# Kernel optimization log

Hardware: AMD Instinct MI355X
Metric: run time of the kernel (lower is better)

The kernel has to match this reference:

```python
import jax, jax.numpy as jnp
import numpy as np

N = 50000      # nodes
E = 800000     # edges (avg degree 16)
F_IN = 32
H = 64         # hidden_features
E_DIM = 16     # edge_dim
C_OUT = 40
L = 2          # num_layers
G = 64         # graphs in batch
BN_EPS = 1e-5
GEN_EPS = 1e-7  # PyG GENConv message eps


def setup_inputs() -> dict:
    key = jax.random.key(0)
    ks = jax.random.split(key, 12)
    s = 0.05
    inp = {}
    inp["x"] = jax.random.normal(ks[0], (N, F_IN), jnp.float32)
    inp["edge_index"] = jax.random.randint(ks[1], (2, E), 0, N)
    inp["edge_attr"] = jax.random.normal(ks[2], (E, E_DIM), jnp.float32)
    inp["batch"] = jnp.sort(jax.random.randint(ks[3], (N,), 0, G))
    # input linear
    inp["lin_in_w"] = jax.random.normal(ks[4], (F_IN, H), jnp.float32) * s
    inp["lin_in_b"] = jnp.zeros((H,), jnp.float32)
    # per-layer DeepGCNLayer norm (BatchNorm affine)
    inp["norm_gamma"] = jnp.ones((L, H), jnp.float32)
    inp["norm_beta"] = jnp.zeros((L, H), jnp.float32)
    # per-layer GENConv params
    inp["edge_w"] = jax.random.normal(ks[5], (L, E_DIM, H), jnp.float32) * s
    inp["edge_b"] = jnp.zeros((L, H), jnp.float32)
    inp["t"] = jnp.ones((L,), jnp.float32)  # learned softmax temperature
    inp["mlp_w1"] = jax.random.normal(ks[6], (L, H, 2 * H), jnp.float32) * s
    inp["mlp_b1"] = jnp.zeros((L, 2 * H), jnp.float32)
    inp["mlp_gamma"] = jnp.ones((L, 2 * H), jnp.float32)
    inp["mlp_beta"] = jnp.zeros((L, 2 * H), jnp.float32)
    inp["mlp_w2"] = jax.random.normal(ks[7], (L, 2 * H, H), jnp.float32) * s
    inp["mlp_b2"] = jnp.zeros((L, H), jnp.float32)
    # output linear
    inp["lin_out_w"] = jax.random.normal(ks[8], (H, C_OUT), jnp.float32) * s
    inp["lin_out_b"] = jnp.zeros((C_OUT,), jnp.float32)
    return inp


def _batch_norm(x, gamma, beta):
    mu = jnp.mean(x, axis=0)
    var = jnp.var(x, axis=0)
    return (x - mu) * jax.lax.rsqrt(var + BN_EPS) * gamma + beta


def _gen_conv(x, src, dst, e_emb, t, w1, b1, g1, be1, w2, b2):
    # message: relu(x_j + edge_emb) + eps   -> [E, H]
    m = jax.nn.relu(x[src] + e_emb) + GEN_EPS
    # softmax aggregation over destination neighborhoods with temperature t
    logits = m * t
    seg_max = jax.ops.segment_max(logits, dst, num_segments=N)      # [N, H]
    ex = jnp.exp(logits - seg_max[dst])                              # [E, H]
    denom = jax.ops.segment_sum(ex, dst, num_segments=N)            # [N, H]
    agg = jax.ops.segment_sum(ex * m, dst, num_segments=N) / (denom + 1e-16)
    # root add, then GENConv MLP: Linear(H,2H) -> BN -> ReLU -> Linear(2H,H)
    out = agg + x
    h = out @ w1 + b1
    h = jax.nn.relu(_batch_norm(h, g1, be1))
    return h @ w2 + b2


def reference(x, edge_index, edge_attr, batch, lin_in_w, lin_in_b,
              norm_gamma, norm_beta, edge_w, edge_b, t,
              mlp_w1, mlp_b1, mlp_gamma, mlp_beta, mlp_w2, mlp_b2,
              lin_out_w, lin_out_b):
    src, dst = edge_index[0], edge_index[1]
    h = x @ lin_in_w + lin_in_b                                      # [N, H]
    for l in range(L):
        # DeepGCNLayer res+ : norm -> act -> (dropout p=0) -> conv, residual add
        z = jax.nn.relu(_batch_norm(h, norm_gamma[l], norm_beta[l]))
        e_emb = edge_attr @ edge_w[l] + edge_b[l]                    # [E, H]
        c = _gen_conv(z, src, dst, e_emb, t[l], mlp_w1[l], mlp_b1[l],
                      mlp_gamma[l], mlp_beta[l], mlp_w2[l], mlp_b2[l])
        h = h + c
    # global mean pool per graph
    sums = jax.ops.segment_sum(h, batch, num_segments=G)             # [G, H]
    counts = jax.ops.segment_sum(jnp.ones((N, 1), h.dtype), batch, num_segments=G)
    pooled = sums / jnp.maximum(counts, 1.0)
    out = jax.nn.relu(pooled) @ lin_out_w + lin_out_b                # [G, C_OUT]
    return out
```

## Files before the change

kernel.cpp:

```cpp
#include <hip/hip_runtime.h>

#define N_NODES 50000
#define N_EDGES 800000
#define F_INP   32
#define HDIM    64
#define EDIM    16
#define COUT    40
#define NGRAPH  64
#define LDS_STRIDE 18

__global__ void hist_kernel(const int* __restrict__ dst, int* __restrict__ cnt, int E) {
    int e = blockIdx.x * 256 + threadIdx.x;
    if (e < E) atomicAdd(&cnt[dst[e]], 1);
}

__global__ void scan_part_kernel(const int* __restrict__ cnt, int* __restrict__ bsum, int n) {
    __shared__ int red[256];
    int tid = threadIdx.x;
    int idx = blockIdx.x * 256 + tid;
    red[tid] = (idx < n) ? cnt[idx] : 0;
    __syncthreads();
    for (int off = 128; off > 0; off >>= 1) {
        if (tid < off) red[tid] += red[tid + off];
        __syncthreads();
    }
    if (tid == 0) bsum[blockIdx.x] = red[0];
}

__global__ void scan_top_kernel(int* __restrict__ bsum, int nb) {
    __shared__ int tmp[256];
    int tid = threadIdx.x;
    int v = (tid < nb) ? bsum[tid] : 0;
    tmp[tid] = v;
    __syncthreads();
    for (int off = 1; off < 256; off <<= 1) {
        int x = (tid >= off) ? tmp[tid - off] : 0;
        __syncthreads();
        tmp[tid] += x;
        __syncthreads();
    }
    if (tid < nb) bsum[tid] = tmp[tid] - v;
}

__global__ void scan_apply_kernel(const int* __restrict__ cnt, const int* __restrict__ bsum,
                                  int* __restrict__ offsets, int* __restrict__ cursor, int n) {
    __shared__ int tmp[256];
    int tid = threadIdx.x;
    int idx = blockIdx.x * 256 + tid;
    int v = (idx < n) ? cnt[idx] : 0;
    tmp[tid] = v;
    __syncthreads();
    for (int off = 1; off < 256; off <<= 1) {
        int x = (tid >= off) ? tmp[tid - off] : 0;
        __syncthreads();
        tmp[tid] += x;
        __syncthreads();
    }
    int excl = tmp[tid] - v + bsum[blockIdx.x];
    if (idx < n) { offsets[idx] = excl; cursor[idx] = excl; }
    if (idx == n - 1) offsets[n] = excl + v;
}

__global__ void scatter_kernel(const int* __restrict__ dst, const int* __restrict__ src,
                               int* __restrict__ cursor, int* __restrict__ sorted,
                               int* __restrict__ dsts, int* __restrict__ srcs, int E) {
    int e = blockIdx.x * 256 + threadIdx.x;
    if (e < E) {
        int d = dst[e];
        int p = atomicAdd(&cursor[d], 1);
        sorted[p] = e;
        dsts[p]   = d;
        srcs[p]   = src[e];
    }
}

__global__ void gstart_kernel(const int* __restrict__ batch, int* __restrict__ gstart,
                              int N, int G) {
    int n = blockIdx.x * 256 + threadIdx.x;
    if (n >= N) return;
    int g  = batch[n];
    int gp = (n == 0) ? -1 : batch[n - 1];
    for (int gg = gp + 1; gg <= g; gg++) gstart[gg] = n;
    if (n == N - 1) {
        for (int gg = g + 1; gg <= G; gg++) gstart[gg] = N;
    }
}

__global__ void lin_in_kernel(const float* __restrict__ x, const float* __restrict__ W,
                              const float* __restrict__ b, float* __restrict__ h, int N) {
    int tid = threadIdx.x;
    int c = tid & 63;
    float w[F_INP];
#pragma unroll
    for (int k = 0; k < F_INP; k++) w[k] = W[k * HDIM + c];
    int node = blockIdx.x * 4 + (tid >> 6);
    if (node >= N) return;
    const float4* xr = (const float4*)(x + (size_t)node * F_INP);
    float acc = b[c];
#pragma unroll
    for (int k4 = 0; k4 < F_INP / 4; k4++) {
        float4 xv = xr[k4];
        acc += xv.x * w[k4 * 4 + 0] + xv.y * w[k4 * 4 + 1]
             + xv.z * w[k4 * 4 + 2] + xv.w * w[k4 * 4 + 3];
    }
    h[(size_t)node * HDIM + c] = acc;
}

template <int C>
__global__ void bn_stats_kernel(const float* __restrict__ x, float* __restrict__ stats, int N) {
    const int RPB = 256 / C;
    int tid = threadIdx.x;
    int c = tid % C;
    int row0 = blockIdx.x * RPB + tid / C;
    int stride = gridDim.x * RPB;
    float s = 0.f, ss = 0.f;
    for (int r = row0; r < N; r += stride) {
        float v = x[(size_t)r * C + c];
        s += v; ss += v * v;
    }
    __shared__ float ls[256], lss[256];
    ls[tid] = s; lss[tid] = ss;
    __syncthreads();
    if (tid < C) {
        for (int k = 1; k < RPB; k++) { s += ls[tid + k * C]; ss += lss[tid + k * C]; }
        atomicAdd(&stats[c], s);
        atomicAdd(&stats[C + c], ss);
    }
}

__global__ __launch_bounds__(256) void edge_agg_kernel(
        const float* __restrict__ h, const float* __restrict__ ea,
        const int* __restrict__ sorted, const int* __restrict__ dsts,
        const int* __restrict__ srcs,
        const float* __restrict__ We, const float* __restrict__ be,
        const float* __restrict__ tptr, const float* __restrict__ stats,
        const float* __restrict__ gamma, const float* __restrict__ beta,
        float* __restrict__ num, float* __restrict__ den) {
    __shared__ float sA[4 * 64 * LDS_STRIDE];
    int tid = threadIdx.x;
    int c  = tid & 63;
    int wv = tid >> 6;
    float inv = 1.0f / (float)N_NODES;
    float mu  = stats[c] * inv;
    float var = stats[HDIM + c] * inv - mu * mu;
    float sc  = rsqrtf(var + 1e-5f) * gamma[c];
    float sb  = beta[c] - mu * sc;
    float w[EDIM];
#pragma unroll
    for (int k = 0; k < EDIM; k++) w[k] = We[k * HDIM + c];
    float bc = be[c];
    float tl2 = (*tptr) * 1.4426950408889634f;

    int p = (blockIdx.x * 4 + wv) * 64 + c;
    int d_own = dsts[p];
    int s_own = srcs[p];
    int e     = sorted[p];
    float* myrow = &sA[(wv * 64 + c) * LDS_STRIDE];
    {
        const float4* ar = (const float4*)(ea + (size_t)e * EDIM);
        float4 a0 = ar[0], a1 = ar[1], a2 = ar[2], a3 = ar[3];
        myrow[0]=a0.x;  myrow[1]=a0.y;  myrow[2]=a0.z;  myrow[3]=a0.w;
        myrow[4]=a1.x;  myrow[5]=a1.y;  myrow[6]=a1.z;  myrow[7]=a1.w;
        myrow[8]=a2.x;  myrow[9]=a2.y;  myrow[10]=a2.z; myrow[11]=a2.w;
        myrow[12]=a3.x; myrow[13]=a3.y; myrow[14]=a3.z; myrow[15]=a3.w;
    }
    __syncthreads();

    const float* wrow = &sA[(size_t)wv * 64 * LDS_STRIDE];
    float nacc = 0.f, dacc = 0.f;
    int cur_d = __builtin_amdgcn_readlane(d_own, 0);
    for (int jj = 0; jj < 64; jj += 8) {
        float hv[8];
#pragma unroll
        for (int u = 0; u < 8; u++) {
            int su = __builtin_amdgcn_readlane(s_own, jj + u);
            hv[u] = h[(size_t)su * HDIM + c];
        }
#pragma unroll
        for (int u = 0; u < 8; u++) {
            int du = __builtin_amdgcn_readlane(d_own, jj + u);
            if (du != cur_d) {
                atomicAdd(&num[(size_t)cur_d * HDIM + c], nacc);
                atomicAdd(&den[(size_t)cur_d * HDIM + c], dacc);
                nacc = 0.f; dacc = 0.f;
                cur_d = du;
            }
            const float2* arow = (const float2*)&wrow[(jj + u) * LDS_STRIDE];
            float acc = bc;
#pragma unroll
            for (int k2 = 0; k2 < 8; k2++) {
                float2 av = arow[k2];
                acc += av.x * w[2 * k2] + av.y * w[2 * k2 + 1];
            }
            float zv = fmaxf(hv[u] * sc + sb, 0.f);
            float m  = fmaxf(zv + acc, 0.f) + 1e-7f;
            float ex = exp2f(m * tl2);
            dacc += ex;
            nacc += ex * m;
        }
    }
    atomicAdd(&num[(size_t)cur_d * HDIM + c], nacc);
    atomicAdd(&den[(size_t)cur_d * HDIM + c], dacc);
}

__global__ __launch_bounds__(256) void mlp1_kernel(
        float* __restrict__ num, float* __restrict__ den,
        const float* __restrict__ h, const float* __restrict__ stats,
        const float* __restrict__ gamma, const float* __restrict__ beta,
        const float* __restrict__ W1, const float* __restrict__ b1,
        float* __restrict__ h1, int N) {
    __shared__ float sW[HDIM * 128];
    __shared__ float srow[32 * 65];
    int tid = threadIdx.x;
    for (int i = tid; i < HDIM * 128; i += 256) sW[i] = W1[i];
    int base = blockIdx.x * 32;
    {
        int cc = tid & 63;
        float inv = 1.0f / (float)N_NODES;
        float mu  = stats[cc] * inv;
        float var = stats[HDIM + cc] * inv - mu * mu;
        float rs  = rsqrtf(var + 1e-5f);
        float ga  = gamma[cc], bb = beta[cc];
        for (int i = tid; i < 32 * HDIM; i += 256) {
            int r = i >> 6;
            int node = base + r;
            float v = 0.f;
            if (node < N) {
                size_t idx = (size_t)node * HDIM + cc;
                float hv = h[idx];
                float z  = fmaxf((hv - mu) * rs * ga + bb, 0.f);
                float nu = num[idx], de = den[idx];
                num[idx] = 0.f; den[idx] = 0.f;
                v = nu / (de + 1e-16f) + z;
            }
            srow[r * 65 + cc] = v;
        }
    }
    __syncthreads();
    int tx = tid & 31;
    int ty = tid >> 5;
    float acc[4][4];
    float b0 = b1[4 * tx], bb1 = b1[4 * tx + 1], b2v = b1[4 * tx + 2], b3 = b1[4 * tx + 3];
#pragma unroll
    for (int j = 0; j < 4; j++) { acc[j][0] = b0; acc[j][1] = bb1; acc[j][2] = b2v; acc[j][3] = b3; }
#pragma unroll 8
    for (int k = 0; k < HDIM; k++) {
        float4 wv = *(const float4*)&sW[k * 128 + 4 * tx];
        float r0 = srow[(ty * 4 + 0) * 65 + k];
        float r1 = srow[(ty * 4 + 1) * 65 + k];
        float r2 = srow[(ty * 4 + 2) * 65 + k];
        float r3 = srow[(ty * 4 + 3) * 65 + k];
        acc[0][0] += r0 * wv.x; acc[0][1] += r0 * wv.y; acc[0][2] += r0 * wv.z; acc[0][3] += r0 * wv.w;
        acc[1][0] += r1 * wv.x; acc[1][1] += r1 * wv.y; acc[1][2] += r1 * wv.z; acc[1][3] += r1 * wv.w;
        acc[2][0] += r2 * wv.x; acc[2][1] += r2 * wv.y; acc[2][2] += r2 * wv.z; acc[2][3] += r2 * wv.w;
        acc[3][0] += r3 * wv.x; acc[3][1] += r3 * wv.y; acc[3][2] += r3 * wv.z; acc[3][3] += r3 * wv.w;
    }
#pragma unroll
    for (int j = 0; j < 4; j++) {
        int node = base + ty * 4 + j;
        if (node < N)
            *(float4*)&h1[(size_t)node * 128 + 4 * tx] =
                make_float4(acc[j][0], acc[j][1], acc[j][2], acc[j][3]);
    }
}

__global__ __launch_bounds__(256) void mlp2_kernel(
        const float* __restrict__ h1, const float* __restrict__ stats,
        const float* __restrict__ mg, const float* __restrict__ mb,
        const float* __restrict__ W2, const float* __restrict__ b2,
        float* __restrict__ h, int N) {
    __shared__ float sW[128 * HDIM];
    __shared__ float sact[32 * 129];
    __shared__ float sbn[4 * 128];
    int tid = threadIdx.x;
    for (int i = tid; i < 128 * HDIM; i += 256) sW[i] = W2[i];
    if (tid < 128) {
        float inv = 1.0f / (float)N;
        float mu  = stats[tid] * inv;
        float var = stats[128 + tid] * inv - mu * mu;
        sbn[tid]       = mu;
        sbn[128 + tid] = rsqrtf(var + 1e-5f);
        sbn[256 + tid] = mg[tid];
        sbn[384 + tid] = mb[tid];
    }
    __syncthreads();
    int base = blockIdx.x * 32;
    for (int i = tid; i < 32 * 128; i += 256) {
        int r = i >> 7, o = i & 127;
        int node = base + r;
        float v = 0.f;
        if (node < N) {
            v = h1[(size_t)node * 128 + o];
            v = fmaxf((v - sbn[o]) * sbn[128 + o] * sbn[256 + o] + sbn[384 + o], 0.f);
        }
        sact[r * 129 + o] = v;
    }
    __syncthreads();
    int tx = tid & 15;
    int ty = tid >> 4;
    float acc[2][4];
    float b0 = b2[4 * tx], bb1 = b2[4 * tx + 1], b2v = b2[4 * tx + 2], b3 = b2[4 * tx + 3];
    acc[0][0] = b0; acc[0][1] = bb1; acc[0][2] = b2v; acc[0][3] = b3;
    acc[1][0] = b0; acc[1][1] = bb1; acc[1][2] = b2v; acc[1][3] = b3;
#pragma unroll 8
    for (int k = 0; k < 128; k++) {
        float4 wv = *(const float4*)&sW[k * HDIM + 4 * tx];
        float r0 = sact[(ty * 2 + 0) * 129 + k];
        float r1 = sact[(ty * 2 + 1) * 129 + k];
        acc[0][0] += r0 * wv.x; acc[0][1] += r0 * wv.y; acc[0][2] += r0 * wv.z; acc[0][3] += r0 * wv.w;
        acc[1][0] += r1 * wv.x; acc[1][1] += r1 * wv.y; acc[1][2] += r1 * wv.z; acc[1][3] += r1 * wv.w;
    }
#pragma unroll
    for (int j = 0; j < 2; j++) {
        int node = base + ty * 2 + j;
        if (node < N) {
            float4* p = (float4*)&h[(size_t)node * HDIM + 4 * tx];
            float4 old = *p;
            *p = make_float4(old.x + acc[j][0], old.y + acc[j][1],
                             old.z + acc[j][2], old.w + acc[j][3]);
        }
    }
}

__global__ void pool_out_kernel(const float* __restrict__ h, const int* __restrict__ gstart,
                                const float* __restrict__ Wo, const float* __restrict__ bo,
                                float* __restrict__ out, int N) {
    __shared__ float sp[HDIM];
    __shared__ float red[256];
    __shared__ float sW[HDIM * COUT];
    int g = blockIdx.x;
    int tid = threadIdx.x;
    for (int i = tid; i < HDIM * COUT; i += 256) sW[i] = Wo[i];
    int beg = gstart[g], end = gstart[g + 1];
    int c = tid & 63, r0 = tid >> 6;
    float s = 0.f;
    for (int r = beg + r0; r < end; r += 4) s += h[(size_t)r * HDIM + c];
    red[tid] = s;
    __syncthreads();
    if (tid < HDIM) {
        s = red[tid] + red[tid + 64] + red[tid + 128] + red[tid + 192];
        float cnt = (float)(end - beg);
        float pooled = s / fmaxf(cnt, 1.0f);
        sp[tid] = fmaxf(pooled, 0.0f);
    }
    __syncthreads();
    if (tid < COUT) {
        float acc = bo[tid];
#pragma unroll
        for (int k = 0; k < HDIM; k++) acc += sp[k] * sW[k * COUT + tid];
        out[g * COUT + tid] = acc;
    }
}

extern "C" void kernel_launch(void* const* d_in, const int* in_sizes, int n_in,
                              void* d_out, int out_size, void* d_ws, size_t ws_size,
                              hipStream_t stream) {
    (void)in_sizes; (void)n_in; (void)out_size; (void)ws_size;
    const float* x          = (const float*)d_in[0];
    const int*   eidx       = (const int*)  d_in[1];
    const float* eattr      = (const float*)d_in[2];
    const int*   batch      = (const int*)  d_in[3];
    const float* lin_in_w   = (const float*)d_in[4];
    const float* lin_in_b   = (const float*)d_in[5];
    const float* norm_gamma = (const float*)d_in[6];
    const float* norm_beta  = (const float*)d_in[7];
    const float* edge_w     = (const float*)d_in[8];
    const float* edge_b     = (const float*)d_in[9];
    const float* tparam     = (const float*)d_in[10];
    const float* mlp_w1     = (const float*)d_in[11];
    const float* mlp_b1     = (const float*)d_in[12];
    const float* mlp_gamma  = (const float*)d_in[13];
    const float* mlp_beta   = (const float*)d_in[14];
    const float* mlp_w2     = (const float*)d_in[15];
    const float* mlp_b2     = (const float*)d_in[16];
    const float* lin_out_w  = (const float*)d_in[17];
    const float* lin_out_b  = (const float*)d_in[18];
    float* out = (float*)d_out;

    const int* src = eidx;
    const int* dst = eidx + N_EDGES;

    char* ws = (char*)d_ws;
    size_t off = 0;
    auto alloc = [&](size_t bytes) -> char* {
        char* p = ws + off;
        off = (off + bytes + 255) & ~(size_t)255;
        return p;
    };
    int*   cnt     = (int*)  alloc((size_t)N_NODES * 4);
    float* statsA0 = (float*)alloc(128 * 4);
    float* statsB0 = (float*)alloc(256 * 4);
    float* statsA1 = (float*)alloc(128 * 4);
    float* statsB1 = (float*)alloc(256 * 4);
    size_t zero_bytes = off;
    int*   bsum    = (int*)  alloc(256 * 4);
    int*   offsets = (int*)  alloc((size_t)(N_NODES + 1) * 4);
    int*   cursor  = (int*)  alloc((size_t)N_NODES * 4);
    int*   sorted  = (int*)  alloc((size_t)N_EDGES * 4);
    int*   dsts    = (int*)  alloc((size_t)N_EDGES * 4);
    int*   srcs    = (int*)  alloc((size_t)N_EDGES * 4);
    int*   gstart  = (int*)  alloc((size_t)(NGRAPH + 1) * 4);
    float* h       = (float*)alloc((size_t)N_NODES * HDIM * 4);
    float* num     = (float*)alloc((size_t)N_NODES * HDIM * 4);
    float* den     = (float*)alloc((size_t)N_NODES * HDIM * 4);
    float* h1      = (float*)alloc((size_t)N_NODES * 2 * HDIM * 4);

    hipMemsetAsync(d_ws, 0, zero_bytes, stream);
    hipMemsetAsync(num, 0, (size_t)N_NODES * HDIM * 4 * 2, stream);

    const int NB = (N_NODES + 255) / 256;
    hist_kernel      <<<(N_EDGES + 255) / 256, 256, 0, stream>>>(dst, cnt, N_EDGES);
    scan_part_kernel <<<NB, 256, 0, stream>>>(cnt, bsum, N_NODES);
    scan_top_kernel  <<<1, 256, 0, stream>>>(bsum, NB);
    scan_apply_kernel<<<NB, 256, 0, stream>>>(cnt, bsum, offsets, cursor, N_NODES);
    scatter_kernel   <<<(N_EDGES + 255) / 256, 256, 0, stream>>>(dst, src, cursor, sorted, dsts, srcs, N_EDGES);
    gstart_kernel    <<<NB, 256, 0, stream>>>(batch, gstart, N_NODES, NGRAPH);
    lin_in_kernel    <<<(N_NODES + 3) / 4, 256, 0, stream>>>(x, lin_in_w, lin_in_b, h, N_NODES);

    const int AGG_BLOCKS = N_EDGES / 256;

    float* statsA[2] = { statsA0, statsA1 };
    float* statsB[2] = { statsB0, statsB1 };
    for (int l = 0; l < 2; l++) {
        bn_stats_kernel<64><<<256, 256, 0, stream>>>(h, statsA[l], N_NODES);
        edge_agg_kernel<<<AGG_BLOCKS, 256, 0, stream>>>(
            h, eattr, sorted, dsts, srcs,
            edge_w + (size_t)l * EDIM * HDIM, edge_b + l * HDIM,
            tparam + l, statsA[l], norm_gamma + l * HDIM, norm_beta + l * HDIM,
            num, den);
        mlp1_kernel<<<(N_NODES + 31) / 32, 256, 0, stream>>>(
            num, den, h, statsA[l], norm_gamma + l * HDIM, norm_beta + l * HDIM,
            mlp_w1 + (size_t)l * HDIM * 2 * HDIM, mlp_b1 + l * 2 * HDIM, h1, N_NODES);
        bn_stats_kernel<128><<<256, 256, 0, stream>>>(h1, statsB[l], N_NODES);
        mlp2_kernel<<<(N_NODES + 31) / 32, 256, 0, stream>>>(
            h1, statsB[l], mlp_gamma + l * 2 * HDIM, mlp_beta + l * 2 * HDIM,
            mlp_w2 + (size_t)l * 2 * HDIM * HDIM, mlp_b2 + l * HDIM, h, N_NODES);
    }
    pool_out_kernel<<<NGRAPH, 256, 0, stream>>>(h, gstart, lin_out_w, lin_out_b, out, N_NODES);
}
```

Measured before the change: 654.4 us.

## Pack sorted edge metadata into int4 and precompute segment boundary ballot mask

The scatter kernel now writes one int4 record per sorted edge (dst, src, edge id) instead of three separate int arrays, so the aggregation kernel gets its metadata with a single vector load. Segment boundaries are found once per wavefront with a shuffle and ballot, which replaces the per-edge readlane comparison. The edge-embedding dot product uses packed 2-wide float vectors to encourage packed FMA, and the outer loop is kept rolled to limit register pressure. The int4 layout carries an unused padding word, which adds write traffic in the scatter kernel.

```diff
diff --git a/kernel.cpp b/kernel.cpp
--- a/kernel.cpp
+++ b/kernel.cpp
@@ -9,6 +9,8 @@
 #define NGRAPH  64
 #define LDS_STRIDE 18
 
+typedef float v2f __attribute__((ext_vector_type(2)));
+
 __global__ void hist_kernel(const int* __restrict__ dst, int* __restrict__ cnt, int E) {
     int e = blockIdx.x * 256 + threadIdx.x;
     if (e < E) atomicAdd(&cnt[dst[e]], 1);
@@ -62,15 +64,12 @@
 }
 
 __global__ void scatter_kernel(const int* __restrict__ dst, const int* __restrict__ src,
-                               int* __restrict__ cursor, int* __restrict__ sorted,
-                               int* __restrict__ dsts, int* __restrict__ srcs, int E) {
+                               int* __restrict__ cursor, int4* __restrict__ edge4, int E) {
     int e = blockIdx.x * 256 + threadIdx.x;
     if (e < E) {
         int d = dst[e];
         int p = atomicAdd(&cursor[d], 1);
-        sorted[p] = e;
-        dsts[p]   = d;
-        srcs[p]   = src[e];
+        edge4[p] = make_int4(d, src[e], e, 0);
     }
 }
 
@@ -130,8 +129,7 @@
 
 __global__ __launch_bounds__(256) void edge_agg_kernel(
         const float* __restrict__ h, const float* __restrict__ ea,
-        const int* __restrict__ sorted, const int* __restrict__ dsts,
-        const int* __restrict__ srcs,
+        const int4* __restrict__ edge4,
         const float* __restrict__ We, const float* __restrict__ be,
         const float* __restrict__ tptr, const float* __restrict__ stats,
         const float* __restrict__ gamma, const float* __restrict__ beta,
@@ -145,16 +143,20 @@
     float var = stats[HDIM + c] * inv - mu * mu;
     float sc  = rsqrtf(var + 1e-5f) * gamma[c];
     float sb  = beta[c] - mu * sc;
-    float w[EDIM];
-#pragma unroll
-    for (int k = 0; k < EDIM; k++) w[k] = We[k * HDIM + c];
+    v2f w2[8];
+#pragma unroll
+    for (int k = 0; k < 8; k++) {
+        w2[k].x = We[(2 * k) * HDIM + c];
+        w2[k].y = We[(2 * k + 1) * HDIM + c];
+    }
     float bc = be[c];
     float tl2 = (*tptr) * 1.4426950408889634f;
 
     int p = (blockIdx.x * 4 + wv) * 64 + c;
-    int d_own = dsts[p];
-    int s_own = srcs[p];
-    int e     = sorted[p];
+    int4 pk = edge4[p];
+    int d_own = pk.x;
+    int s_own = pk.y;
+    int e     = pk.z;
     float* myrow = &sA[(wv * 64 + c) * LDS_STRIDE];
     {
         const float4* ar = (const float4*)(ea + (size_t)e * EDIM);
@@ -164,11 +166,14 @@
         myrow[8]=a2.x;  myrow[9]=a2.y;  myrow[10]=a2.z; myrow[11]=a2.w;
         myrow[12]=a3.x; myrow[13]=a3.y; myrow[14]=a3.z; myrow[15]=a3.w;
     }
+    int dprev = __shfl_up(d_own, 1);
+    unsigned long long bmask = __ballot(c > 0 && d_own != dprev);
     __syncthreads();
 
     const float* wrow = &sA[(size_t)wv * 64 * LDS_STRIDE];
     float nacc = 0.f, dacc = 0.f;
     int cur_d = __builtin_amdgcn_readlane(d_own, 0);
+#pragma unroll 1
     for (int jj = 0; jj < 64; jj += 8) {
         float hv[8];
 #pragma unroll
@@ -178,20 +183,18 @@
         }
 #pragma unroll
         for (int u = 0; u < 8; u++) {
-            int du = __builtin_amdgcn_readlane(d_own, jj + u);
-            if (du != cur_d) {
+            if (bmask & (1ull << (jj + u))) {
                 atomicAdd(&num[(size_t)cur_d * HDIM + c], nacc);
                 atomicAdd(&den[(size_t)cur_d * HDIM + c], dacc);
                 nacc = 0.f; dacc = 0.f;
-                cur_d = du;
+                cur_d = __builtin_amdgcn_readlane(d_own, jj + u);
             }
-            const float2* arow = (const float2*)&wrow[(jj + u) * LDS_STRIDE];
-            float acc = bc;
-#pragma unroll
-            for (int k2 = 0; k2 < 8; k2++) {
-                float2 av = arow[k2];
-                acc += av.x * w[2 * k2] + av.y * w[2 * k2 + 1];
-            }
+            const v2f* arow = (const v2f*)&wrow[(jj + u) * LDS_STRIDE];
+            v2f acc2 = {bc, 0.f};
+#pragma unroll
+            for (int k2 = 0; k2 < 8; k2++)
+                acc2 += arow[k2] * w2[k2];
+            float acc = acc2.x + acc2.y;
             float zv = fmaxf(hv[u] * sc + sb, 0.f);
             float m  = fmaxf(zv + acc, 0.f) + 1e-7f;
             float ex = exp2f(m * tl2);
@@ -396,9 +399,7 @@
     int*   bsum    = (int*)  alloc(256 * 4);
     int*   offsets = (int*)  alloc((size_t)(N_NODES + 1) * 4);
     int*   cursor  = (int*)  alloc((size_t)N_NODES * 4);
-    int*   sorted  = (int*)  alloc((size_t)N_EDGES * 4);
-    int*   dsts    = (int*)  alloc((size_t)N_EDGES * 4);
-    int*   srcs    = (int*)  alloc((size_t)N_EDGES * 4);
+    int4*  edge4   = (int4*) alloc((size_t)N_EDGES * 16);
     int*   gstart  = (int*)  alloc((size_t)(NGRAPH + 1) * 4);
     float* h       = (float*)alloc((size_t)N_NODES * HDIM * 4);
     float* num     = (float*)alloc((size_t)N_NODES * HDIM * 4);
@@ -413,7 +414,7 @@
     scan_part_kernel <<<NB, 256, 0, stream>>>(cnt, bsum, N_NODES);
     scan_top_kernel  <<<1, 256, 0, stream>>>(bsum, NB);
     scan_apply_kernel<<<NB, 256, 0, stream>>>(cnt, bsum, offsets, cursor, N_NODES);
-    scatter_kernel   <<<(N_EDGES + 255) / 256, 256, 0, stream>>>(dst, src, cursor, sorted, dsts, srcs, N_EDGES);
+    scatter_kernel   <<<(N_EDGES + 255) / 256, 256, 0, stream>>>(dst, src, cursor, edge4, N_EDGES);
     gstart_kernel    <<<NB, 256, 0, stream>>>(batch, gstart, N_NODES, NGRAPH);
     lin_in_kernel    <<<(N_NODES + 3) / 4, 256, 0, stream>>>(x, lin_in_w, lin_in_b, h, N_NODES);
 
@@ -424,7 +425,7 @@
     for (int l = 0; l < 2; l++) {
         bn_stats_kernel<64><<<256, 256, 0, stream>>>(h, statsA[l], N_NODES);
         edge_agg_kernel<<<AGG_BLOCKS, 256, 0, stream>>>(
-            h, eattr, sorted, dsts, srcs,
+            h, eattr, edge4,
             edge_w + (size_t)l * EDIM * HDIM, edge_b + l * HDIM,
             tparam + l, statsA[l], norm_gamma + l * HDIM, norm_beta + l * HDIM,
             num, den);
```

Measured after the change: 631.8 us. 1.04x faster.
